# Optimization experiments

Hardware: AMD Instinct MI355X
Metric: run time of the kernel (lower is better)

## Reference

```python
import jax, jax.numpy as jnp
import numpy as np

N, E, H, L, B = 200000, 800000, 128, 4, 2000  # nodes, directed edges, hidden, layers, graphs
ATOM, BOND = 28, 6


def setup_inputs() -> dict:
    key = jax.random.key(0)
    ks = jax.random.split(key, 12)
    h = jax.random.normal(ks[0], (N, ATOM), jnp.float32)
    e = jax.random.normal(ks[1], (E, BOND), jnp.float32)
    # paired directed edges: edge 2i = (u->v), edge 2i+1 = (v->u), so rev(k) = k ^ 1
    u = jax.random.randint(ks[2], (E // 2,), 0, N)
    v = jax.random.randint(ks[3], (E // 2,), 0, N)
    src = jnp.stack([u, v], axis=1).reshape(-1)
    dst = jnp.stack([v, u], axis=1).reshape(-1)
    graph_id = jnp.sort(jax.random.randint(ks[4], (N,), 0, B))
    s = 1.0 / np.sqrt(H).astype(np.float32)
    W_emb = jax.random.normal(ks[5], (ATOM, H), jnp.float32) * (1.0 / np.sqrt(ATOM))
    W_init = jax.random.normal(ks[6], (H + BOND, H), jnp.float32) * s
    b_init = jnp.zeros((H,), jnp.float32)
    W_layers = jax.random.normal(ks[7], (L, H, H), jnp.float32) * s
    b_layers = jnp.zeros((L, H), jnp.float32)
    W_ro = jax.random.normal(ks[8], (H, H), jnp.float32) * s
    W_pred = jax.random.normal(ks[9], (H, 1), jnp.float32) * s
    b_pred = jnp.zeros((1,), jnp.float32)
    snorm_n = jnp.ones((N, 1), jnp.float32)
    snorm_e = jnp.ones((E, 1), jnp.float32)
    return dict(h=h, e=e, W_emb=W_emb, W_init=W_init, b_init=b_init,
                W_layers=W_layers, b_layers=b_layers, W_ro=W_ro,
                W_pred=W_pred, b_pred=b_pred, src=src, dst=dst,
                graph_id=graph_id, snorm_n=snorm_n, snorm_e=snorm_e)


def reference(h, e, W_emb, W_init, b_init, W_layers, b_layers, W_ro,
              W_pred, b_pred, src, dst, graph_id, snorm_n, snorm_e):
    n_nodes = h.shape[0]
    n_edges = src.shape[0]
    rev = jnp.arange(n_edges) ^ 1  # paired reverse-edge index
    # node embedding (dropout is identity at p=0); x kept as residual input per source
    x = h @ W_emb  # [N, H]
    # init_message_func: per-edge relu(Linear(cat(h_src, e)))
    he = jax.nn.relu(jnp.concatenate([x[src], e], axis=1) @ W_init + b_init)  # [E, H]
    # D-MPNN layers: aggregate incoming edge states at src node, exclude reverse edge,
    # linear + relu (norms disabled in this config), outer residual add
    n_layers = W_layers.shape[0]
    for l in range(n_layers):
        agg = jax.ops.segment_sum(he, dst, num_segments=n_nodes)  # sum of edge states into each node
        m = agg[src] - he[rev]                                    # exclude reverse edge
        he = jax.nn.relu(m @ W_layers[l] + b_layers[l]) + he      # residual
    # update_all(copy_edge, sum): node state = sum of incoming edge states
    h_out = jax.ops.segment_sum(he, dst, num_segments=n_nodes)  # [N, H]
    h_ro = h_out @ W_ro                                          # linear_ro (no bias)
    # readout == 'sum': per-graph sum of node states
    hg = jax.ops.segment_sum(h_ro, graph_id, num_segments=B)     # [B, H]
    return hg @ W_pred + b_pred                                  # [B, 1]
```

## Files before the change

kernel.cpp:

```cpp
#include <hip/hip_runtime.h>
#include <hip/hip_bf16.h>

#define H 128
#define ATOM 28
#define BOND 6
#define NLAYERS 4
#define TE 32
#define LW 136
#define LKI 72
#define LE 40
typedef unsigned short US;
typedef unsigned int UI;
typedef short bf16x8 __attribute__((ext_vector_type(8)));
typedef float f32x4 __attribute__((ext_vector_type(4)));
#define MFMA(a,b,c) __builtin_amdgcn_mfma_f32_16x16x32_bf16((a),(b),(c),0,0,0)

__device__ __forceinline__ float bf2f(US u) {
    union { unsigned int i; float f; } v; v.i = ((unsigned int)u) << 16; return v.f;
}
__device__ __forceinline__ US f2bf(float f) {
    union { float f; unsigned int i; } v; v.f = f;
    unsigned int r = v.i + 0x7FFF + ((v.i >> 16) & 1);
    return (US)(r >> 16);
}
__device__ __forceinline__ float in_ld(const void* p, long long i, int bf) {
    return bf ? bf2f(((const US*)p)[i]) : ((const float*)p)[i];
}

__global__ void detect_kernel(const void* snorm, int* flag) {
    const US* u = (const US*)snorm;
    *flag = (u[0] == 0x3F80 && u[2] == 0x3F80) ? 1 : 0;
}

__global__ void fail_kernel(void* out, int nB, float val, const int* flag) {
    int i = blockIdx.x * 256 + threadIdx.x;
    if (i < nB) {
        if (*flag) ((US*)out)[i] = f2bf(val);
        else       ((float*)out)[i] = val;
    }
}

__global__ void build_wt(const void* __restrict__ W_emb, const void* __restrict__ W_init,
                         const int* __restrict__ flag, US* __restrict__ WtG) {
    int bf = *flag;
    int k = blockIdx.x;
    int c = threadIdx.x;
    float v = 0.f;
    if (k < ATOM) {
        for (int j = 0; j < H; ++j)
            v += in_ld(W_emb, k * H + j, bf) * in_ld(W_init, (long long)j * H + c, bf);
    }
    WtG[c * 64 + k] = f2bf(v);
}

__global__ void build_w2x(const void* __restrict__ W_init, const int* __restrict__ flag,
                          US* __restrict__ W2x) {
    int bf = *flag;
    int k = blockIdx.x;
    int c = threadIdx.x;
    float v = (k < BOND) ? in_ld(W_init, (long long)(H + k) * H + c, bf) : 0.f;
    W2x[c * 32 + k] = f2bf(v);
}

__global__ void build_wtL(const void* __restrict__ W_layers, const int* __restrict__ flag,
                          US* __restrict__ WtL) {
    int bf = *flag;
    int l = blockIdx.x >> 7, n = blockIdx.x & 127;
    int k = threadIdx.x;
    long long si = (long long)l * H * H + (long long)k * H + n;
    WtL[((long long)l * H + n) * H + k] = bf ? ((const US*)W_layers)[si]
                                             : f2bf(((const float*)W_layers)[si]);
}

__global__ void build_wp(const void* __restrict__ W_ro, const void* __restrict__ W_pred,
                         const int* __restrict__ flag, float* __restrict__ wp) {
    int bf = *flag;
    int c = threadIdx.x;
    float s = 0.f;
    for (int j = 0; j < H; ++j)
        s += in_ld(W_ro, (long long)c * H + j, bf) * in_ld(W_pred, j, bf);
    wp[c] = s;
}

__global__ void hist_kernel(const int* __restrict__ dst, int* __restrict__ cnt, int nE) {
    int k = blockIdx.x * 256 + threadIdx.x;
    if (k < nE) atomicAdd(&cnt[dst[k]], 1);
}

__global__ __launch_bounds__(256) void scan1(const int* __restrict__ cnt,
                                             int* __restrict__ rowptr,
                                             int* __restrict__ partials, int nN) {
    __shared__ int sd[256];
    int t = threadIdx.x;
    int base = blockIdx.x * 1024 + t * 4;
    int l0 = (base + 0 < nN) ? cnt[base + 0] : 0;
    int l1 = (base + 1 < nN) ? cnt[base + 1] : 0;
    int l2 = (base + 2 < nN) ? cnt[base + 2] : 0;
    int l3 = (base + 3 < nN) ? cnt[base + 3] : 0;
    int s = l0 + l1 + l2 + l3;
    sd[t] = s; __syncthreads();
    for (int off = 1; off < 256; off <<= 1) {
        int v = (t >= off) ? sd[t - off] : 0;
        __syncthreads();
        sd[t] += v;
        __syncthreads();
    }
    int excl = sd[t] - s;
    if (base + 0 < nN) rowptr[base + 0] = excl;
    if (base + 1 < nN) rowptr[base + 1] = excl + l0;
    if (base + 2 < nN) rowptr[base + 2] = excl + l0 + l1;
    if (base + 3 < nN) rowptr[base + 3] = excl + l0 + l1 + l2;
    if (t == 255) partials[blockIdx.x] = sd[255];
}

__global__ __launch_bounds__(256) void scan2(const int* __restrict__ partials,
                                             int* __restrict__ blockoff, int SB) {
    __shared__ int sd[256];
    int t = threadIdx.x;
    int v = (t < SB) ? partials[t] : 0;
    sd[t] = v; __syncthreads();
    for (int off = 1; off < 256; off <<= 1) {
        int x = (t >= off) ? sd[t - off] : 0;
        __syncthreads();
        sd[t] += x;
        __syncthreads();
    }
    blockoff[t] = sd[t] - v;
}

__global__ void scan3(int* __restrict__ rowptr, int* __restrict__ cursor,
                      const int* __restrict__ blockoff, int nN, int nE) {
    int i = blockIdx.x * 256 + threadIdx.x;
    if (i < nN) {
        int v = rowptr[i] + blockoff[i >> 10];
        rowptr[i] = v;
        cursor[i] = v;
    }
    if (i == 0) rowptr[nN] = nE;
}

__global__ void fill_kernel(const int* __restrict__ dst, int* __restrict__ cursor,
                            int* __restrict__ ein, int nE) {
    int k = blockIdx.x * 256 + threadIdx.x;
    if (k < nE) {
        int pos = atomicAdd(&cursor[dst[k]], 1);
        ein[pos] = k;
    }
}

__global__ __launch_bounds__(256) void agg_gather(
    const US* __restrict__ he, const int* __restrict__ rowptr,
    const int* __restrict__ ein, US* __restrict__ agg, int nN) {
    int n = blockIdx.x * 4 + (threadIdx.x >> 6);
    int lane = threadIdx.x & 63;
    if (n >= nN) return;
    const UI* heU = (const UI*)he;
    int s = rowptr[n], epos = rowptr[n + 1];
    float f0 = 0.f, f1 = 0.f;
    int idx = s;
    for (; idx + 4 <= epos; idx += 4) {
        int e0 = ein[idx], e1 = ein[idx + 1], e2 = ein[idx + 2], e3 = ein[idx + 3];
        UI u0 = heU[(long long)e0 * 64 + lane];
        UI u1 = heU[(long long)e1 * 64 + lane];
        UI u2 = heU[(long long)e2 * 64 + lane];
        UI u3 = heU[(long long)e3 * 64 + lane];
        f0 += bf2f((US)(u0 & 0xFFFF)) + bf2f((US)(u1 & 0xFFFF))
            + bf2f((US)(u2 & 0xFFFF)) + bf2f((US)(u3 & 0xFFFF));
        f1 += bf2f((US)(u0 >> 16)) + bf2f((US)(u1 >> 16))
            + bf2f((US)(u2 >> 16)) + bf2f((US)(u3 >> 16));
    }
    for (; idx < epos; ++idx) {
        UI u = heU[(long long)ein[idx] * 64 + lane];
        f0 += bf2f((US)(u & 0xFFFF));
        f1 += bf2f((US)(u >> 16));
    }
    ((UI*)agg)[(long long)n * 64 + lane] = (UI)f2bf(f0) | ((UI)f2bf(f1) << 16);
}

__global__ __launch_bounds__(256) void node_sum(
    const float* __restrict__ s, const int* __restrict__ rowptr,
    const int* __restrict__ ein, const int* __restrict__ graph_id,
    float* __restrict__ hgS, int nN) {
    __shared__ int sg[256];
    __shared__ float sv[256];
    int tid = threadIdx.x;
    int n = blockIdx.x * 256 + tid;
    float acc = 0.f;
    int g = -1;
    if (n < nN) {
        g = graph_id[n];
        int e0 = rowptr[n], e1 = rowptr[n + 1];
        for (int idx = e0; idx < e1; ++idx) acc += s[ein[idx]];
    }
    sg[tid] = g; sv[tid] = acc;
    __syncthreads();
    if (tid == 0) {
        int cg = sg[0]; float a = sv[0];
        for (int i = 1; i < 256; ++i) {
            if (sg[i] == cg) a += sv[i];
            else {
                if (cg >= 0) unsafeAtomicAdd(&hgS[cg], a);
                cg = sg[i]; a = sv[i];
            }
        }
        if (cg >= 0) unsafeAtomicAdd(&hgS[cg], a);
    }
}

__global__ __launch_bounds__(256) void agg_dot(
    const US* __restrict__ agg, const float* __restrict__ wp,
    const int* __restrict__ graph_id, float* __restrict__ hgS, int nN) {
    __shared__ float sv[4];
    __shared__ int sg[4];
    int wave = threadIdx.x >> 6, lane = threadIdx.x & 63;
    int n = blockIdx.x * 4 + wave;
    bool valid = n < nN;
    float v = 0.f;
    if (valid) {
        UI u = ((const UI*)agg)[(long long)n * 64 + lane];
        v = bf2f((US)(u & 0xFFFF)) * wp[2 * lane]
          + bf2f((US)(u >> 16)) * wp[2 * lane + 1];
        #pragma unroll
        for (int off = 32; off > 0; off >>= 1) v += __shfl_down(v, off);
    }
    if (lane == 0) {
        sv[wave] = valid ? v : 0.f;
        sg[wave] = valid ? graph_id[n] : -1;
    }
    __syncthreads();
    if (threadIdx.x == 0) {
        int cg = sg[0]; float acc = sv[0];
        #pragma unroll
        for (int w = 1; w < 4; ++w) {
            if (sg[w] == cg) acc += sv[w];
            else {
                if (cg >= 0) unsafeAtomicAdd(&hgS[cg], acc);
                cg = sg[w]; acc = sv[w];
            }
        }
        if (cg >= 0) unsafeAtomicAdd(&hgS[cg], acc);
    }
}

__global__ void finish_kernel(const float* __restrict__ hgS, const void* __restrict__ b_pred,
                              const int* __restrict__ flag, void* __restrict__ out, int nB) {
    int bf = *flag;
    int i = blockIdx.x * 256 + threadIdx.x;
    if (i < nB) {
        float r = hgS[i] + in_ld(b_pred, 0, bf);
        if (bf) ((US*)out)[i] = f2bf(r);
        else    ((float*)out)[i] = r;
    }
}

__global__ __launch_bounds__(256) void scatter_cas(
    const US* __restrict__ he, const int* __restrict__ dst,
    US* __restrict__ agg, long long totalPairs) {
    const UI* heU = (const UI*)he;
    UI* aggU = (UI*)agg;
    long long i = (long long)blockIdx.x * blockDim.x + threadIdx.x;
    long long stride = (long long)gridDim.x * blockDim.x;
    for (; i < totalPairs; i += stride) {
        int k = (int)(i >> 6);
        int jp = (int)(i & 63);
        UI pv = heU[i];
        float v0 = bf2f((US)(pv & 0xFFFF));
        float v1 = bf2f((US)(pv >> 16));
        UI* addr = aggU + (long long)dst[k] * 64 + jp;
        UI old = *addr, assumed;
        do {
            assumed = old;
            UI nv = (UI)f2bf(bf2f((US)(assumed & 0xFFFF)) + v0)
                  | ((UI)f2bf(bf2f((US)(assumed >> 16)) + v1) << 16);
            old = atomicCAS(addr, assumed, nv);
        } while (old != assumed);
    }
}

__global__ __launch_bounds__(256) void node_gemm(
    const void* __restrict__ h, const US* __restrict__ WtG,
    const int* __restrict__ flag, US* __restrict__ xn, int nN) {
    __shared__ __align__(16) US sA[TE * LKI];
    __shared__ __align__(16) US sO[TE * LW];
    const int bf = *flag;
    const int tid = threadIdx.x;
    const int wave = tid >> 6, lane = tid & 63;
    const int quad = lane >> 4, l16 = lane & 15;
    const int ncol0 = wave * 32;
    bf16x8 bw[2][2];
    #pragma unroll
    for (int i = 0; i < 2; ++i)
        #pragma unroll
        for (int c = 0; c < 2; ++c)
            bw[i][c] = *(const bf16x8*)&WtG[(ncol0 + c * 16 + l16) * 64 + i * 32 + quad * 8];

    UI* sAU = (UI*)sA;
    for (int i = tid; i < TE * (LKI / 2); i += 256) sAU[i] = 0u;

    int ntiles = (nN + TE - 1) / TE;
    for (int t = blockIdx.x; t < ntiles; t += gridDim.x) {
        int n0 = t * TE;
        __syncthreads();
        for (int i = tid; i < TE * 14; i += 256) {
            int r = i / 14, u = i % 14;
            int n = n0 + r;
            UI v = 0;
            if (n < nN) {
                if (bf) v = ((const UI*)h)[(long long)n * 14 + u];
                else {
                    const float* hF = (const float*)h + (long long)n * ATOM + 2 * u;
                    v = (UI)f2bf(hF[0]) | ((UI)f2bf(hF[1]) << 16);
                }
            }
            sAU[r * (LKI / 2) + u] = v;
        }
        __syncthreads();

        f32x4 acc00 = {0,0,0,0}, acc01 = {0,0,0,0}, acc10 = {0,0,0,0}, acc11 = {0,0,0,0};
        #pragma unroll
        for (int i = 0; i < 2; ++i) {
            int kb = i * 32 + quad * 8;
            bf16x8 a0 = *(const bf16x8*)&sA[l16 * LKI + kb];
            bf16x8 a1 = *(const bf16x8*)&sA[(l16 + 16) * LKI + kb];
            acc00 = MFMA(a0, bw[i][0], acc00);
            acc01 = MFMA(a0, bw[i][1], acc01);
            acc10 = MFMA(a1, bw[i][0], acc10);
            acc11 = MFMA(a1, bw[i][1], acc11);
        }
        #pragma unroll
        for (int mt = 0; mt < 2; ++mt)
            #pragma unroll
            for (int reg = 0; reg < 4; ++reg) {
                int row = mt * 16 + quad * 4 + reg;
                #pragma unroll
                for (int nt = 0; nt < 2; ++nt) {
                    float a = mt ? (nt ? acc11[reg] : acc10[reg])
                                 : (nt ? acc01[reg] : acc00[reg]);
                    sO[row * LW + ncol0 + nt * 16 + l16] = f2bf(a);
                }
            }
        int row2 = lane >> 1, half = lane & 1;
        int cbase = ncol0 + half * 16;
        int n = n0 + row2;
        if (n < nN) {
            uint4 o0 = *(const uint4*)&sO[row2 * LW + cbase];
            uint4 o1 = *(const uint4*)&sO[row2 * LW + cbase + 8];
            uint4* dst4 = (uint4*)(xn + (long long)n * H + cbase);
            dst4[0] = o0; dst4[1] = o1;
        }
    }
}

__global__ __launch_bounds__(256) void init_edge(
    const void* __restrict__ e, const US* __restrict__ xn,
    const US* __restrict__ W2x, const void* __restrict__ b_init,
    const int* __restrict__ src, const int* __restrict__ flag,
    US* __restrict__ he, int nE) {
    __shared__ __align__(16) US sE[2][TE * LE];
    __shared__ __align__(16) US sX[2][TE * LW];
    const int bf = *flag;
    const int tid = threadIdx.x;
    const int wave = tid >> 6, lane = tid & 63;
    const int quad = lane >> 4, l16 = lane & 15;
    const int ncol0 = wave * 32;
    float rb0 = in_ld(b_init, ncol0 + l16, bf);
    float rb1 = in_ld(b_init, ncol0 + 16 + l16, bf);
    bf16x8 bw2[2];
    #pragma unroll
    for (int c = 0; c < 2; ++c)
        bw2[c] = *(const bf16x8*)&W2x[(ncol0 + c * 16 + l16) * 32 + quad * 8];

    for (int b = 0; b < 2; ++b) {
        UI* z = (UI*)sE[b];
        for (int i = tid; i < TE * (LE / 2); i += 256) z[i] = 0u;
    }

    const int r0 = tid >> 4, q0 = tid & 15;
    const int er = tid / 3, eu = tid - er * 3;
    int ntiles = nE / TE;
    int t = blockIdx.x;
    UI ve = 0; uint4 vx0, vx1;
    if (t < ntiles) {
        int k0 = t * TE;
        if (tid < 96) {
            if (bf) ve = ((const UI*)e)[(long long)(k0 + er) * 3 + eu];
            else {
                const float* eF = (const float*)e + (long long)(k0 + er) * BOND + 2 * eu;
                ve = (UI)f2bf(eF[0]) | ((UI)f2bf(eF[1]) << 16);
            }
        }
        int s0 = src[k0 + r0], s1 = src[k0 + r0 + 16];
        vx0 = ((const uint4*)(xn + (long long)s0 * H))[q0];
        vx1 = ((const uint4*)(xn + (long long)s1 * H))[q0];
    }
    int buf = 0;
    for (; t < ntiles; t += gridDim.x, buf ^= 1) {
        int k0 = t * TE;
        if (tid < 96) ((UI*)sE[buf])[er * (LE / 2) + eu] = ve;
        *(uint4*)&sX[buf][r0 * LW + q0 * 8] = vx0;
        *(uint4*)&sX[buf][(r0 + 16) * LW + q0 * 8] = vx1;
        __syncthreads();
        int tn = t + gridDim.x;
        if (tn < ntiles) {
            int kn = tn * TE;
            if (tid < 96) {
                if (bf) ve = ((const UI*)e)[(long long)(kn + er) * 3 + eu];
                else {
                    const float* eF = (const float*)e + (long long)(kn + er) * BOND + 2 * eu;
                    ve = (UI)f2bf(eF[0]) | ((UI)f2bf(eF[1]) << 16);
                }
            }
            int s0 = src[kn + r0], s1 = src[kn + r0 + 16];
            vx0 = ((const uint4*)(xn + (long long)s0 * H))[q0];
            vx1 = ((const uint4*)(xn + (long long)s1 * H))[q0];
        }

        f32x4 acc00 = {0,0,0,0}, acc01 = {0,0,0,0}, acc10 = {0,0,0,0}, acc11 = {0,0,0,0};
        {
            int kb = quad * 8;
            bf16x8 a0 = *(const bf16x8*)&sE[buf][l16 * LE + kb];
            bf16x8 a1 = *(const bf16x8*)&sE[buf][(l16 + 16) * LE + kb];
            acc00 = MFMA(a0, bw2[0], acc00);
            acc01 = MFMA(a0, bw2[1], acc01);
            acc10 = MFMA(a1, bw2[0], acc10);
            acc11 = MFMA(a1, bw2[1], acc11);
        }
        #pragma unroll
        for (int mt = 0; mt < 2; ++mt)
            #pragma unroll
            for (int reg = 0; reg < 4; ++reg) {
                int row = mt * 16 + quad * 4 + reg;
                #pragma unroll
                for (int nt = 0; nt < 2; ++nt) {
                    float a = mt ? (nt ? acc11[reg] : acc10[reg])
                                 : (nt ? acc01[reg] : acc00[reg]);
                    int col = ncol0 + nt * 16 + l16;
                    float v = fmaxf(a + bf2f(sX[buf][row * LW + col]) + (nt ? rb1 : rb0), 0.f);
                    sX[buf][row * LW + col] = f2bf(v);
                }
            }
        int row2 = lane >> 1, half = lane & 1;
        int cbase = ncol0 + half * 16;
        uint4 o0 = *(const uint4*)&sX[buf][row2 * LW + cbase];
        uint4 o1 = *(const uint4*)&sX[buf][row2 * LW + cbase + 8];
        uint4* dst4 = (uint4*)(he + (long long)(k0 + row2) * H + cbase);
        dst4[0] = o0; dst4[1] = o1;
    }
}

__global__ __launch_bounds__(256) void mfma_layer(
    const US* __restrict__ agg, const int* __restrict__ src,
    const US* __restrict__ WtL, const void* __restrict__ b_layers,
    int layer, const int* __restrict__ flag, US* __restrict__ he,
    const float* __restrict__ wp, float* __restrict__ sOut, int nE) {
    __shared__ __align__(16) US sHe[2][TE * LW];
    __shared__ __align__(16) US sAgg[2][TE * LW];
    __shared__ float sS[4][TE];
    const int bf = *flag;
    const int tid = threadIdx.x;
    const int wave = tid >> 6, lane = tid & 63;
    const int quad = lane >> 4, l16 = lane & 15;
    const int ncol0 = wave * 32;
    float rb0 = in_ld(b_layers, (long long)layer * H + ncol0 + l16, bf);
    float rb1 = in_ld(b_layers, (long long)layer * H + ncol0 + 16 + l16, bf);
    const bool last = (sOut != nullptr);
    float w0 = 0.f, w1 = 0.f;
    if (last) { w0 = wp[ncol0 + l16]; w1 = wp[ncol0 + 16 + l16]; }
    const US* Wl = WtL + (size_t)layer * H * H;
    bf16x8 bw[4][2];
    #pragma unroll
    for (int i = 0; i < 4; ++i)
        #pragma unroll
        for (int c = 0; c < 2; ++c)
            bw[i][c] = *(const bf16x8*)&Wl[(ncol0 + c * 16 + l16) * H + i * 32 + quad * 8];

    const int r0 = tid >> 4, q0 = tid & 15;
    int ntiles = nE / TE;
    int t = blockIdx.x;
    uint4 vh0, vh1, va0, va1;
    if (t < ntiles) {
        int k0 = t * TE;
        const uint4* heG = (const uint4*)(he + (long long)k0 * H);
        vh0 = heG[tid]; vh1 = heG[tid + 256];
        int s0 = src[k0 + r0], s1 = src[k0 + r0 + 16];
        va0 = ((const uint4*)(agg + (long long)s0 * H))[q0];
        va1 = ((const uint4*)(agg + (long long)s1 * H))[q0];
    }
    int buf = 0;
    for (; t < ntiles; t += gridDim.x, buf ^= 1) {
        int k0 = t * TE;
        *(uint4*)&sHe[buf][r0 * LW + q0 * 8] = vh0;
        *(uint4*)&sHe[buf][(r0 + 16) * LW + q0 * 8] = vh1;
        *(uint4*)&sAgg[buf][r0 * LW + q0 * 8] = va0;
        *(uint4*)&sAgg[buf][(r0 + 16) * LW + q0 * 8] = va1;
        __syncthreads();
        int tn = t + gridDim.x;
        if (tn < ntiles) {
            int kn = tn * TE;
            const uint4* heG = (const uint4*)(he + (long long)kn * H);
            vh0 = heG[tid]; vh1 = heG[tid + 256];
            int s0 = src[kn + r0], s1 = src[kn + r0 + 16];
            va0 = ((const uint4*)(agg + (long long)s0 * H))[q0];
            va1 = ((const uint4*)(agg + (long long)s1 * H))[q0];
        }

        f32x4 g1a = {0,0,0,0}, g1b = {0,0,0,0}, g1c = {0,0,0,0}, g1d = {0,0,0,0};
        f32x4 g2a = {0,0,0,0}, g2b = {0,0,0,0}, g2c = {0,0,0,0}, g2d = {0,0,0,0};
        #pragma unroll
        for (int i = 0; i < 4; ++i) {
            int kb = i * 32 + quad * 8;
            bf16x8 aA0 = *(const bf16x8*)&sAgg[buf][l16 * LW + kb];
            bf16x8 aA1 = *(const bf16x8*)&sAgg[buf][(l16 + 16) * LW + kb];
            bf16x8 aH0 = *(const bf16x8*)&sHe[buf][l16 * LW + kb];
            bf16x8 aH1 = *(const bf16x8*)&sHe[buf][(l16 + 16) * LW + kb];
            g1a = MFMA(aA0, bw[i][0], g1a); g1b = MFMA(aA0, bw[i][1], g1b);
            g1c = MFMA(aA1, bw[i][0], g1c); g1d = MFMA(aA1, bw[i][1], g1d);
            g2a = MFMA(aH0, bw[i][0], g2a); g2b = MFMA(aH0, bw[i][1], g2b);
            g2c = MFMA(aH1, bw[i][0], g2c); g2d = MFMA(aH1, bw[i][1], g2d);
        }
        __syncthreads();

        if (!last) {
            #pragma unroll
            for (int mt = 0; mt < 2; ++mt)
                #pragma unroll
                for (int reg = 0; reg < 4; ++reg) {
                    int row = mt * 16 + quad * 4 + reg;
                    #pragma unroll
                    for (int nt = 0; nt < 2; ++nt) {
                        float g1 = mt ? (nt ? g1d[reg] : g1c[reg])
                                      : (nt ? g1b[reg] : g1a[reg]);
                        float g2 = mt ? (nt ? g2d[reg ^ 1] : g2c[reg ^ 1])
                                      : (nt ? g2b[reg ^ 1] : g2a[reg ^ 1]);
                        int col = ncol0 + nt * 16 + l16;
                        float v = fmaxf(g1 - g2 + (nt ? rb1 : rb0), 0.f)
                                + bf2f(sHe[buf][row * LW + col]);
                        sAgg[buf][row * LW + col] = f2bf(v);
                    }
                }
            int row2 = lane >> 1, half = lane & 1;
            int cbase = ncol0 + half * 16;
            uint4 o0 = *(const uint4*)&sAgg[buf][row2 * LW + cbase];
            uint4 o1 = *(const uint4*)&sAgg[buf][row2 * LW + cbase + 8];
            uint4* dst4 = (uint4*)(he + (long long)(k0 + row2) * H + cbase);
            dst4[0] = o0; dst4[1] = o1;
        } else {
            float prow[8];
            #pragma unroll
            for (int mt = 0; mt < 2; ++mt)
                #pragma unroll
                for (int reg = 0; reg < 4; ++reg) {
                    int row = mt * 16 + quad * 4 + reg;
                    float acc = 0.f;
                    #pragma unroll
                    for (int nt = 0; nt < 2; ++nt) {
                        float g1 = mt ? (nt ? g1d[reg] : g1c[reg])
                                      : (nt ? g1b[reg] : g1a[reg]);
                        float g2 = mt ? (nt ? g2d[reg ^ 1] : g2c[reg ^ 1])
                                      : (nt ? g2b[reg ^ 1] : g2a[reg ^ 1]);
                        int col = ncol0 + nt * 16 + l16;
                        float v = fmaxf(g1 - g2 + (nt ? rb1 : rb0), 0.f)
                                + bf2f(sHe[buf][row * LW + col]);
                        acc += v * (nt ? w1 : w0);
                    }
                    prow[mt * 4 + reg] = acc;
                }
            #pragma unroll
            for (int off = 1; off < 16; off <<= 1)
                #pragma unroll
                for (int j = 0; j < 8; ++j)
                    prow[j] += __shfl_xor(prow[j], off);
            if (l16 == 0) {
                #pragma unroll
                for (int j = 0; j < 8; ++j) {
                    int row = (j >> 2) * 16 + quad * 4 + (j & 3);
                    sS[wave][row] = prow[j];
                }
            }
            __syncthreads();
            if (tid < TE) {
                float sv = sS[0][tid] + sS[1][tid] + sS[2][tid] + sS[3][tid];
                sOut[k0 + tid] = sv;
            }
        }
    }
}

extern "C" void kernel_launch(void* const* d_in, const int* in_sizes, int n_in,
                              void* d_out, int out_size, void* d_ws, size_t ws_size,
                              hipStream_t stream) {
    const void* h        = d_in[0];
    const void* e        = d_in[1];
    const void* W_emb    = d_in[2];
    const void* W_init   = d_in[3];
    const void* b_init   = d_in[4];
    const void* W_layers = d_in[5];
    const void* b_layers = d_in[6];
    const void* W_ro     = d_in[7];
    const void* W_pred   = d_in[8];
    const void* b_pred   = d_in[9];
    const int*  src      = (const int*)d_in[10];
    const int*  dst      = (const int*)d_in[11];
    const int*  graph_id = (const int*)d_in[12];
    const void* snorm_n  = d_in[13];

    int nN = in_sizes[0] / ATOM;
    int nE = in_sizes[1] / BOND;
    int nB = out_size;
    int SB = (nN + 1023) / 1024;

    size_t off = 0;
    auto alloc = [&](size_t bytes) { size_t o = off; off = (off + bytes + 255) & ~(size_t)255; return o; };
    size_t o_flag = alloc(256);
    size_t o_wt   = alloc((size_t)H * 64 * sizeof(US));
    size_t o_w2x  = alloc((size_t)H * 32 * sizeof(US));
    size_t o_wtL  = alloc((size_t)NLAYERS * H * H * sizeof(US));
    size_t o_wp   = alloc((size_t)H * sizeof(float));
    size_t o_hgs  = alloc((size_t)nB * sizeof(float));
    size_t o_cnt  = alloc((size_t)nN * sizeof(int));
    size_t o_rp   = alloc((size_t)(nN + 1) * sizeof(int));
    size_t o_cur  = alloc((size_t)nN * sizeof(int));
    size_t o_par  = alloc(256 * sizeof(int));
    size_t o_boff = alloc(256 * sizeof(int));
    size_t o_ein  = alloc((size_t)nE * sizeof(int));
    size_t o_s    = alloc((size_t)nE * sizeof(float));
    size_t o_agg  = alloc((size_t)nN * H * sizeof(US));
    size_t o_he   = alloc((size_t)nE * H * sizeof(US));
    size_t needG  = off;

    char* W = (char*)d_ws;
    int*   flag   = (int*)(W + o_flag);
    US*    WtG    = (US*)(W + o_wt);
    US*    W2x    = (US*)(W + o_w2x);
    US*    WtL    = (US*)(W + o_wtL);
    float* wp     = (float*)(W + o_wp);
    float* hgS    = (float*)(W + o_hgs);
    int*   cnt    = (int*)(W + o_cnt);
    int*   rowptr = (int*)(W + o_rp);
    int*   cursor = (int*)(W + o_cur);
    int*   part   = (int*)(W + o_par);
    int*   boff   = (int*)(W + o_boff);
    int*   ein    = (int*)(W + o_ein);
    float* sbuf   = (float*)(W + o_s);
    US*    agg    = (US*)(W + o_agg);
    US*    he     = (US*)(W + o_he);

    detect_kernel<<<1, 1, 0, stream>>>(snorm_n, flag);
    build_wt<<<64, 128, 0, stream>>>(W_emb, W_init, flag, WtG);
    build_w2x<<<32, 128, 0, stream>>>(W_init, flag, W2x);
    build_wtL<<<NLAYERS * H, 128, 0, stream>>>(W_layers, flag, WtL);
    build_wp<<<1, 128, 0, stream>>>(W_ro, W_pred, flag, wp);

    if (ws_size >= needG && SB <= 256) {
        hipMemsetAsync(cnt, 0, (size_t)nN * sizeof(int), stream);
        hist_kernel<<<(nE + 255) / 256, 256, 0, stream>>>(dst, cnt, nE);
        scan1<<<SB, 256, 0, stream>>>(cnt, rowptr, part, nN);
        scan2<<<1, 256, 0, stream>>>(part, boff, SB);
        scan3<<<(nN + 255) / 256, 256, 0, stream>>>(rowptr, cursor, boff, nN, nE);
        fill_kernel<<<(nE + 255) / 256, 256, 0, stream>>>(dst, cursor, ein, nE);

        node_gemm<<<2048, 256, 0, stream>>>(h, WtG, flag, agg , nN);
        init_edge<<<2048, 256, 0, stream>>>(e, agg , W2x, b_init, src, flag, he, nE);
        for (int l = 0; l < NLAYERS; ++l) {
            agg_gather<<<(nN + 3) / 4, 256, 0, stream>>>(he, rowptr, ein, agg, nN);
            float* sArg = (l == NLAYERS - 1) ? sbuf : nullptr;
            mfma_layer<<<2048, 256, 0, stream>>>(agg, src, WtL, b_layers, l, flag, he,
                                                 wp, sArg, nE);
        }
        hipMemsetAsync(hgS, 0, (size_t)nB * sizeof(float), stream);
        node_sum<<<(nN + 255) / 256, 256, 0, stream>>>(sbuf, rowptr, ein, graph_id, hgS, nN);
        finish_kernel<<<(nB + 255) / 256, 256, 0, stream>>>(hgS, b_pred, flag, d_out, nB);
        return;
    }

    size_t off2 = 0;
    auto alloc2 = [&](size_t bytes) { size_t o = off2; off2 = (off2 + bytes + 255) & ~(size_t)255; return o; };
    alloc2(256);
    alloc2((size_t)H * 64 * sizeof(US));
    alloc2((size_t)H * 32 * sizeof(US));
    alloc2((size_t)NLAYERS * H * H * sizeof(US));
    size_t f2_wp  = alloc2((size_t)H * sizeof(float));
    size_t f2_hgs = alloc2((size_t)nB * sizeof(float));
    size_t f2_agg = alloc2((size_t)nN * H * sizeof(US));
    size_t f2_he  = alloc2((size_t)nE * H * sizeof(US));
    size_t needT  = off2;

    if (ws_size >= needT) {
        float* wp2  = (float*)(W + f2_wp);
        float* hgS2 = (float*)(W + f2_hgs);
        US*    agg2 = (US*)(W + f2_agg);
        US*    he2  = (US*)(W + f2_he);
        build_wp<<<1, 128, 0, stream>>>(W_ro, W_pred, flag, wp2);
        node_gemm<<<2048, 256, 0, stream>>>(h, WtG, flag, agg2 , nN);
        init_edge<<<2048, 256, 0, stream>>>(e, agg2, W2x, b_init, src, flag, he2, nE);
        for (int l = 0; l < NLAYERS; ++l) {
            hipMemsetAsync(agg2, 0, (size_t)nN * H * sizeof(US), stream);
            scatter_cas<<<2048, 256, 0, stream>>>(he2, dst, agg2, (long long)nE * (H / 2));
            mfma_layer<<<2048, 256, 0, stream>>>(agg2, src, WtL, b_layers, l, flag, he2,
                                                 wp2, (float*)nullptr, nE);
        }
        hipMemsetAsync(agg2, 0, (size_t)nN * H * sizeof(US), stream);
        scatter_cas<<<2048, 256, 0, stream>>>(he2, dst, agg2, (long long)nE * (H / 2));
        hipMemsetAsync(hgS2, 0, (size_t)nB * sizeof(float), stream);
        agg_dot<<<(nN + 3) / 4, 256, 0, stream>>>(agg2, wp2, graph_id, hgS2, nN);
        finish_kernel<<<(nB + 255) / 256, 256, 0, stream>>>(hgS2, b_pred, flag, d_out, nB);
    } else {
        float val = (float)(ws_size >> 20) * 1e6f;
        fail_kernel<<<(nB + 255) / 256, 256, 0, stream>>>(d_out, nB, val, flag);
    }
}
```

Before: 1.096 ms.

## Vectorize agg gather with 16-byte loads across edges and single-buffer layer LDS

The node aggregation kernel now has each quarter-wave load a full 256-byte edge row as uint4 vectors, so four edges are fetched in parallel, then reduces the partials across quads with shuffles. This replaces the old pattern of one 4-byte load per lane per edge, aiming for wider memory transactions and more loads in flight. The layer kernel drops its double-buffered shared-memory tiles for a single buffer and adds an extra barrier after the writeback. That halves LDS use, which may raise occupancy, but it adds synchronization per tile. A helper for packing two bf16 values is also factored out.

After: 1.065 ms, median of 2. -2.8%, faster.

```diff
diff --git a/kernel.cpp b/kernel.cpp
--- a/kernel.cpp
+++ b/kernel.cpp
@@ -22,6 +22,9 @@
     union { float f; unsigned int i; } v; v.f = f;
     unsigned int r = v.i + 0x7FFF + ((v.i >> 16) & 1);
     return (US)(r >> 16);
+}
+__device__ __forceinline__ UI pack2(float a, float b) {
+    return (UI)f2bf(a) | ((UI)f2bf(b) << 16);
 }
 __device__ __forceinline__ float in_ld(const void* p, long long i, int bf) {
     return bf ? bf2f(((const US*)p)[i]) : ((const float*)p)[i];
@@ -153,28 +156,35 @@
     const int* __restrict__ ein, US* __restrict__ agg, int nN) {
     int n = blockIdx.x * 4 + (threadIdx.x >> 6);
     int lane = threadIdx.x & 63;
+    int quad = lane >> 4, l16 = lane & 15;
     if (n >= nN) return;
-    const UI* heU = (const UI*)he;
+    const uint4* heV = (const uint4*)he;
     int s = rowptr[n], epos = rowptr[n + 1];
-    float f0 = 0.f, f1 = 0.f;
-    int idx = s;
-    for (; idx + 4 <= epos; idx += 4) {
-        int e0 = ein[idx], e1 = ein[idx + 1], e2 = ein[idx + 2], e3 = ein[idx + 3];
-        UI u0 = heU[(long long)e0 * 64 + lane];
-        UI u1 = heU[(long long)e1 * 64 + lane];
-        UI u2 = heU[(long long)e2 * 64 + lane];
-        UI u3 = heU[(long long)e3 * 64 + lane];
-        f0 += bf2f((US)(u0 & 0xFFFF)) + bf2f((US)(u1 & 0xFFFF))
-            + bf2f((US)(u2 & 0xFFFF)) + bf2f((US)(u3 & 0xFFFF));
-        f1 += bf2f((US)(u0 >> 16)) + bf2f((US)(u1 >> 16))
-            + bf2f((US)(u2 >> 16)) + bf2f((US)(u3 >> 16));
-    }
-    for (; idx < epos; ++idx) {
-        UI u = heU[(long long)ein[idx] * 64 + lane];
-        f0 += bf2f((US)(u & 0xFFFF));
-        f1 += bf2f((US)(u >> 16));
-    }
-    ((UI*)agg)[(long long)n * 64 + lane] = (UI)f2bf(f0) | ((UI)f2bf(f1) << 16);
+    float f[8];
+    #pragma unroll
+    for (int j = 0; j < 8; ++j) f[j] = 0.f;
+    for (int idx = s; idx < epos; idx += 4) {
+        int j = idx + quad;
+        if (j < epos) {
+            int e = ein[j];
+            uint4 v = heV[(long long)e * 16 + l16];
+            f[0] += bf2f((US)(v.x & 0xFFFF)); f[1] += bf2f((US)(v.x >> 16));
+            f[2] += bf2f((US)(v.y & 0xFFFF)); f[3] += bf2f((US)(v.y >> 16));
+            f[4] += bf2f((US)(v.z & 0xFFFF)); f[5] += bf2f((US)(v.z >> 16));
+            f[6] += bf2f((US)(v.w & 0xFFFF)); f[7] += bf2f((US)(v.w >> 16));
+        }
+    }
+    #pragma unroll
+    for (int j = 0; j < 8; ++j) {
+        f[j] += __shfl_xor(f[j], 16);
+        f[j] += __shfl_xor(f[j], 32);
+    }
+    if (quad == 0) {
+        uint4 o;
+        o.x = pack2(f[0], f[1]); o.y = pack2(f[2], f[3]);
+        o.z = pack2(f[4], f[5]); o.w = pack2(f[6], f[7]);
+        ((uint4*)agg)[(long long)n * 16 + l16] = o;
+    }
 }
 
 __global__ __launch_bounds__(256) void node_sum(
@@ -309,7 +319,7 @@
                 if (bf) v = ((const UI*)h)[(long long)n * 14 + u];
                 else {
                     const float* hF = (const float*)h + (long long)n * ATOM + 2 * u;
-                    v = (UI)f2bf(hF[0]) | ((UI)f2bf(hF[1]) << 16);
+                    v = pack2(hF[0], hF[1]);
                 }
             }
             sAU[r * (LKI / 2) + u] = v;
@@ -386,7 +396,7 @@
             if (bf) ve = ((const UI*)e)[(long long)(k0 + er) * 3 + eu];
             else {
                 const float* eF = (const float*)e + (long long)(k0 + er) * BOND + 2 * eu;
-                ve = (UI)f2bf(eF[0]) | ((UI)f2bf(eF[1]) << 16);
+                ve = pack2(eF[0], eF[1]);
             }
         }
         int s0 = src[k0 + r0], s1 = src[k0 + r0 + 16];
@@ -407,7 +417,7 @@
                 if (bf) ve = ((const UI*)e)[(long long)(kn + er) * 3 + eu];
                 else {
                     const float* eF = (const float*)e + (long long)(kn + er) * BOND + 2 * eu;
-                    ve = (UI)f2bf(eF[0]) | ((UI)f2bf(eF[1]) << 16);
+                    ve = pack2(eF[0], eF[1]);
                 }
             }
             int s0 = src[kn + r0], s1 = src[kn + r0 + 16];
@@ -453,8 +463,8 @@
     const US* __restrict__ WtL, const void* __restrict__ b_layers,
     int layer, const int* __restrict__ flag, US* __restrict__ he,
     const float* __restrict__ wp, float* __restrict__ sOut, int nE) {
-    __shared__ __align__(16) US sHe[2][TE * LW];
-    __shared__ __align__(16) US sAgg[2][TE * LW];
+    __shared__ __align__(16) US sHe[TE * LW];
+    __shared__ __align__(16) US sAgg[TE * LW];
     __shared__ float sS[4][TE];
     const int bf = *flag;
     const int tid = threadIdx.x;
@@ -486,13 +496,12 @@
         va0 = ((const uint4*)(agg + (long long)s0 * H))[q0];
         va1 = ((const uint4*)(agg + (long long)s1 * H))[q0];
     }
-    int buf = 0;
-    for (; t < ntiles; t += gridDim.x, buf ^= 1) {
+    for (; t < ntiles; t += gridDim.x) {
         int k0 = t * TE;
-        *(uint4*)&sHe[buf][r0 * LW + q0 * 8] = vh0;
-        *(uint4*)&sHe[buf][(r0 + 16) * LW + q0 * 8] = vh1;
-        *(uint4*)&sAgg[buf][r0 * LW + q0 * 8] = va0;
-        *(uint4*)&sAgg[buf][(r0 + 16) * LW + q0 * 8] = va1;
+        *(uint4*)&sHe[r0 * LW + q0 * 8] = vh0;
+        *(uint4*)&sHe[(r0 + 16) * LW + q0 * 8] = vh1;
+        *(uint4*)&sAgg[r0 * LW + q0 * 8] = va0;
+        *(uint4*)&sAgg[(r0 + 16) * LW + q0 * 8] = va1;
         __syncthreads();
         int tn = t + gridDim.x;
         if (tn < ntiles) {
@@ -509,10 +518,10 @@
         #pragma unroll
         for (int i = 0; i < 4; ++i) {
             int kb = i * 32 + quad * 8;
-            bf16x8 aA0 = *(const bf16x8*)&sAgg[buf][l16 * LW + kb];
-            bf16x8 aA1 = *(const bf16x8*)&sAgg[buf][(l16 + 16) * LW + kb];
-            bf16x8 aH0 = *(const bf16x8*)&sHe[buf][l16 * LW + kb];
-            bf16x8 aH1 = *(const bf16x8*)&sHe[buf][(l16 + 16) * LW + kb];
+            bf16x8 aA0 = *(const bf16x8*)&sAgg[l16 * LW + kb];
+            bf16x8 aA1 = *(const bf16x8*)&sAgg[(l16 + 16) * LW + kb];
+            bf16x8 aH0 = *(const bf16x8*)&sHe[l16 * LW + kb];
+            bf16x8 aH1 = *(const bf16x8*)&sHe[(l16 + 16) * LW + kb];
             g1a = MFMA(aA0, bw[i][0], g1a); g1b = MFMA(aA0, bw[i][1], g1b);
             g1c = MFMA(aA1, bw[i][0], g1c); g1d = MFMA(aA1, bw[i][1], g1d);
             g2a = MFMA(aH0, bw[i][0], g2a); g2b = MFMA(aH0, bw[i][1], g2b);
@@ -534,16 +543,17 @@
                                       : (nt ? g2b[reg ^ 1] : g2a[reg ^ 1]);
                         int col = ncol0 + nt * 16 + l16;
                         float v = fmaxf(g1 - g2 + (nt ? rb1 : rb0), 0.f)
-                                + bf2f(sHe[buf][row * LW + col]);
-                        sAgg[buf][row * LW + col] = f2bf(v);
+                                + bf2f(sHe[row * LW + col]);
+                        sAgg[row * LW + col] = f2bf(v);
                     }
                 }
             int row2 = lane >> 1, half = lane & 1;
             int cbase = ncol0 + half * 16;
-            uint4 o0 = *(const uint4*)&sAgg[buf][row2 * LW + cbase];
-            uint4 o1 = *(const uint4*)&sAgg[buf][row2 * LW + cbase + 8];
+            uint4 o0 = *(const uint4*)&sAgg[row2 * LW + cbase];
+            uint4 o1 = *(const uint4*)&sAgg[row2 * LW + cbase + 8];
             uint4* dst4 = (uint4*)(he + (long long)(k0 + row2) * H + cbase);
             dst4[0] = o0; dst4[1] = o1;
+            __syncthreads();
         } else {
             float prow[8];
             #pragma unroll
@@ -560,7 +570,7 @@
                                       : (nt ? g2b[reg ^ 1] : g2a[reg ^ 1]);
                         int col = ncol0 + nt * 16 + l16;
                         float v = fmaxf(g1 - g2 + (nt ? rb1 : rb0), 0.f)
-                                + bf2f(sHe[buf][row * LW + col]);
+                                + bf2f(sHe[row * LW + col]);
                         acc += v * (nt ? w1 : w0);
                     }
                     prow[mt * 4 + reg] = acc;
```
